# Optimization experiments

Measured on AMD Instinct MI355X. Metric: run time of the kernel, lower is better.

Reference implementation:

```python
import jax, jax.numpy as jnp
import numpy as np

B, C, H, W_SP = 16, 128, 28, 28
F, KS, STRIDE, PAD = 128, 3, 1, 1
CHUNK = 4      # filters per chunk for the L1 reduction (limits intermediate size)
EPS = 1e-12


def setup_inputs() -> dict:
    key = jax.random.key(0)
    kx, kw = jax.random.split(key)
    x = jax.random.normal(kx, (B, C, H, W_SP), dtype=jnp.float32)
    # kaiming_normal_: std = sqrt(2 / fan_in), fan_in = C*KS*KS
    std = float(np.sqrt(2.0 / (C * KS * KS)))
    W = jax.random.normal(kw, (F, C, KS, KS), dtype=jnp.float32) * std
    return {"x": x, "W": W}


def _patches(x):
    # im2col: [B, C*KS*KS, h_out, w_out], feature order (c, kh, kw) like torch unfold
    p = jax.lax.conv_general_dilated_patches(
        x, (KS, KS), (STRIDE, STRIDE), [(PAD, PAD), (PAD, PAD)],
        dimension_numbers=('NCHW', 'OIHW', 'NCHW'))
    b, k, ho, wo = p.shape
    return p.reshape(b, k, ho * wo), ho, wo


def reference(x, W):
    P, ho, wo = _patches(x)          # [B, K, L]
    Wc = W.reshape(F, -1)            # [F, K]
    K = Wc.shape[1]

    # Forward value: out = -cdist_L1(W, X_col) = -sum_k |W[f,k] - P[b,k,l]|
    # computed in filter chunks to avoid the full [F, K, B*L] diff tensor.
    Wch = Wc.reshape(F // CHUNK, CHUNK, K)
    def chunk_fn(wc):                # wc: [CHUNK, K]
        return jnp.sum(jnp.abs(wc[None, :, :, None] - P[:, None, :, :]), axis=2)  # [B, CHUNK, L]
    neg_l1 = -jax.lax.map(chunk_fn, Wch)                     # [F//CHUNK, B, CHUNK, L]
    neg_l1 = jnp.transpose(neg_l1, (1, 0, 2, 3)).reshape(P.shape[0], F, -1)  # [B, F, L]

    # Gradient path in original (straight-through): -cdist_L2, via GEMM decomposition.
    d2 = (jnp.sum(Wc * Wc, axis=1)[None, :, None]
          + jnp.sum(P * P, axis=1)[:, None, :]
          - 2.0 * jnp.einsum('fk,bkl->bfl', Wc, P))
    neg_l2 = -jnp.sqrt(jnp.maximum(d2, EPS))

    # value = -L1, gradient flows through -L2 (out.data = out_2.data in torch)
    out = neg_l2 + jax.lax.stop_gradient(neg_l1 - neg_l2)    # [B, F, L]
    return out.reshape(P.shape[0], F, ho, wo)
```

## Files before the change

### kernel.cpp

```cpp
#include <hip/hip_runtime.h>


#define B_    16
#define C_    128
#define HH    28
#define WW    28
#define F_    128
#define L_    (HH * WW)
#define K_    (C_ * 9)
#define M_    (B_ * L_)
#define TM    64
#define BC    4
#define KC    (BC * 9)
#define KP    (KC / 2)
#define SLAB  (B_ * F_ * L_)
#define NMT   (M_ / TM)
#define QS    4096.0f
#define QB    32768.5f

__device__ __forceinline__ unsigned sad16(unsigned a, unsigned b, unsigned c) {
    asm("v_sad_u16 %0, %1, %2, %0" : "+v"(c) : "v"(a), "v"(b));
    return c;
}

__global__ __launch_bounds__(256, 3)
void adder2d_main(const float* __restrict__ x, const float* __restrict__ Wg,
                  float* __restrict__ dst, int nch, int direct) {
    __shared__ __align__(16) unsigned Plq[2][KP][TM];
    __shared__ __align__(16) unsigned Wlq[2][KP][F_];

    const int t    = threadIdx.x;
    const int lane = t & 63;
    const int w    = t >> 6;
    const int tx   = lane & 7;
    const int ty   = lane >> 3;
    const int fw   = 32 * w;
    const int mt   = blockIdx.x, sp = blockIdx.z;
    const int c0   = sp * nch * BC;

    const int m  = mt * TM + lane;
    const int b  = m / L_;
    const int l  = m - b * L_;
    const int ho = l / WW, wo = l - ho * WW;
    int   toff[9];
    float sc[9];
    #pragma unroll
    for (int r = 0; r < 9; ++r) {
        const int dy = r / 3 - 1;
        const int dx = r - (r / 3) * 3 - 1;
        const bool ok = ((unsigned)(ho + dy) < (unsigned)HH) &&
                        ((unsigned)(wo + dx) < (unsigned)WW);
        toff[r] = ok ? (dy * WW + dx) : 0;
        sc[r]   = ok ? QS : 0.0f;
    }
    const float* xb = x + (size_t)b * (C_ * L_) + l;

    const int cp = w >> 1;
    const int r0 = (w & 1) ? 5 : 0;
    const int fW = t >> 1;
    const int pW = t & 1;
    const float* wbase = Wg + (size_t)fW * K_;

    unsigned acc[8][4];
    #pragma unroll
    for (int i = 0; i < 8; ++i)
        #pragma unroll
        for (int j = 0; j < 4; ++j) acc[i][j] = 0u;

    float ppre[10];
    float wpre[18];

    auto loadP = [&](int c8) {
        const float* x1 = xb + (size_t)(c8 + cp) * L_;
        const float* x2 = x1 + 2 * L_;
        #pragma unroll
        for (int i = 0; i < 5; ++i) {
            const int r  = r0 + i;
            const int rr = (r > 8) ? 8 : r;
            ppre[i]     = x1[toff[rr]];
            ppre[5 + i] = x2[toff[rr]];
        }
    };
    auto loadW = [&](int c8) {
        const float* w1 = wbase + (size_t)(c8 + pW) * 9;
        #pragma unroll
        for (int i = 0; i < 9; ++i) {
            wpre[i]     = w1[i];
            wpre[9 + i] = w1[18 + i];
        }
    };

    loadP(c0);
    loadW(c0);

    #pragma unroll 1
    for (int ch = 0; ch < nch; ++ch) {
        const int bufi = ch & 1;
        #pragma unroll
        for (int i = 0; i < 5; ++i) {
            const int r = r0 + i;
            if (r <= 8) {
                const unsigned qlo = (unsigned)__builtin_fmaf(ppre[i],     sc[r], QB);
                const unsigned qhi = (unsigned)__builtin_fmaf(ppre[5 + i], sc[r], QB);
                Plq[bufi][cp * 9 + r][lane] = (qlo & 0xffffu) | (qhi << 16);
            }
        }
        #pragma unroll
        for (int i = 0; i < 9; ++i) {
            const unsigned qlo = (unsigned)__builtin_fmaf(wpre[i],     QS, QB);
            const unsigned qhi = (unsigned)__builtin_fmaf(wpre[9 + i], QS, QB);
            Wlq[bufi][pW * 9 + i][fW] = (qlo & 0xffffu) | (qhi << 16);
        }
        if (ch + 1 < nch) {
            loadP(c0 + (ch + 1) * BC);
            loadW(c0 + (ch + 1) * BC);
        }
        asm volatile("s_waitcnt lgkmcnt(0)" ::: "memory");
        __builtin_amdgcn_s_barrier();
        asm volatile("" ::: "memory");
        __builtin_amdgcn_sched_barrier(0);
        #pragma unroll 6
        for (int kp = 0; kp < KP; ++kp) {
            const uint4 pA = *(const uint4*)&Plq[bufi][kp][tx * 8];
            const uint4 pB = *(const uint4*)&Plq[bufi][kp][tx * 8 + 4];
            const uint4 wA = *(const uint4*)&Wlq[bufi][kp][fw + ty * 4];
            const unsigned pm[8] = {pA.x, pA.y, pA.z, pA.w,
                                    pB.x, pB.y, pB.z, pB.w};
            const unsigned wn[4] = {wA.x, wA.y, wA.z, wA.w};
            #pragma unroll
            for (int i = 0; i < 8; ++i)
                #pragma unroll
                for (int j = 0; j < 4; ++j)
                    acc[i][j] = sad16(pm[i], wn[j], acc[i][j]);
        }
    }

    const int mb = mt * TM + tx * 8;
    const int bI = mb / L_;
    const int lb = mb - bI * L_;
    float* slab = direct ? dst : dst + (size_t)sp * SLAB;
    const float qs = (direct ? -1.0f : 1.0f) / QS;
    #pragma unroll
    for (int j = 0; j < 4; ++j) {
        const int f = fw + ty * 4 + j;
        float* o = &slab[(size_t)(bI * F_ + f) * L_ + lb];
        *(float4*)o       = make_float4(qs * (float)acc[0][j], qs * (float)acc[1][j],
                                        qs * (float)acc[2][j], qs * (float)acc[3][j]);
        *(float4*)(o + 4) = make_float4(qs * (float)acc[4][j], qs * (float)acc[5][j],
                                        qs * (float)acc[6][j], qs * (float)acc[7][j]);
    }
}

__global__ __launch_bounds__(256)
void adder2d_combine(const float* __restrict__ ws, float* __restrict__ out,
                     int nslab) {
    const int i = blockIdx.x * 256 + threadIdx.x;
    float4 r = make_float4(0.0f, 0.0f, 0.0f, 0.0f);
    for (int s = 0; s < nslab; ++s) {
        const float4 p = ((const float4*)(ws + (size_t)s * SLAB))[i];
        r.x += p.x; r.y += p.y; r.z += p.z; r.w += p.w;
    }
    ((float4*)out)[i] = make_float4(-r.x, -r.y, -r.z, -r.w);
}

extern "C" void kernel_launch(void* const* d_in, const int* in_sizes, int n_in,
                              void* d_out, int out_size, void* d_ws, size_t ws_size,
                              hipStream_t stream) {
    const float* x = (const float*)d_in[0];
    const float* W = (const float*)d_in[1];
    float* out = (float*)d_out;
    float* ws  = (float*)d_ws;

    int split = 0;
    if (ws_size >= (size_t)8 * SLAB * sizeof(float))      split = 8;
    else if (ws_size >= (size_t)4 * SLAB * sizeof(float)) split = 4;

    if (split) {
        dim3 grid(NMT, 1, split);
        adder2d_main<<<grid, 256, 0, stream>>>(x, W, ws, (C_ / BC) / split, 0);
        adder2d_combine<<<SLAB / 4 / 256, 256, 0, stream>>>(ws, out, split);
    } else {
        dim3 grid(NMT, 1, 1);
        adder2d_main<<<grid, 256, 0, stream>>>(x, W, out, C_ / BC, 1);
    }
}
```

Before: 113.4 us.

## Use 128-thread blocks with 8x8 per-thread SAD tiles and direct weight loads

Halves the block to two waves and has each thread accumulate an 8x8 tile instead of 8x4, so every LDS read of weights feeds twice as many SAD ops. Each thread now stages a full filter row per chunk with float4 global loads in the chunk loop, with no prefetch into registers. Patch staging now covers all 9 taps per wave. Register use roughly doubles and occupancy drops, and the weight loads are no longer overlapped with compute.

```diff
diff --git a/kernel.cpp b/kernel.cpp
--- a/kernel.cpp
+++ b/kernel.cpp
@@ -23,7 +23,7 @@
     return c;
 }
 
-__global__ __launch_bounds__(256, 3)
+__global__ __launch_bounds__(128, 2)
 void adder2d_main(const float* __restrict__ x, const float* __restrict__ Wg,
                   float* __restrict__ dst, int nch, int direct) {
     __shared__ __align__(16) unsigned Plq[2][KP][TM];
@@ -34,7 +34,7 @@
     const int w    = t >> 6;
     const int tx   = lane & 7;
     const int ty   = lane >> 3;
-    const int fw   = 32 * w;
+    const int fw   = 64 * w;
     const int mt   = blockIdx.x, sp = blockIdx.z;
     const int c0   = sp * nch * BC;
 
@@ -55,82 +55,76 @@
     }
     const float* xb = x + (size_t)b * (C_ * L_) + l;
 
-    const int cp = w >> 1;
-    const int r0 = (w & 1) ? 5 : 0;
-    const int fW = t >> 1;
-    const int pW = t & 1;
-    const float* wbase = Wg + (size_t)fW * K_;
+    const float* wrow = Wg + (size_t)t * K_;
 
-    unsigned acc[8][4];
+    unsigned acc[8][8];
     #pragma unroll
     for (int i = 0; i < 8; ++i)
         #pragma unroll
-        for (int j = 0; j < 4; ++j) acc[i][j] = 0u;
+        for (int j = 0; j < 8; ++j) acc[i][j] = 0u;
 
-    float ppre[10];
-    float wpre[18];
-
+    float ppre[18];
     auto loadP = [&](int c8) {
-        const float* x1 = xb + (size_t)(c8 + cp) * L_;
+        const float* x1 = xb + (size_t)(c8 + w) * L_;
         const float* x2 = x1 + 2 * L_;
         #pragma unroll
-        for (int i = 0; i < 5; ++i) {
-            const int r  = r0 + i;
-            const int rr = (r > 8) ? 8 : r;
-            ppre[i]     = x1[toff[rr]];
-            ppre[5 + i] = x2[toff[rr]];
-        }
-    };
-    auto loadW = [&](int c8) {
-        const float* w1 = wbase + (size_t)(c8 + pW) * 9;
-        #pragma unroll
-        for (int i = 0; i < 9; ++i) {
-            wpre[i]     = w1[i];
-            wpre[9 + i] = w1[18 + i];
+        for (int r = 0; r < 9; ++r) {
+            ppre[r]     = x1[toff[r]];
+            ppre[9 + r] = x2[toff[r]];
         }
     };
 
     loadP(c0);
-    loadW(c0);
 
     #pragma unroll 1
     for (int ch = 0; ch < nch; ++ch) {
         const int bufi = ch & 1;
+        const int c8 = c0 + ch * BC;
         #pragma unroll
-        for (int i = 0; i < 5; ++i) {
-            const int r = r0 + i;
-            if (r <= 8) {
-                const unsigned qlo = (unsigned)__builtin_fmaf(ppre[i],     sc[r], QB);
-                const unsigned qhi = (unsigned)__builtin_fmaf(ppre[5 + i], sc[r], QB);
-                Plq[bufi][cp * 9 + r][lane] = (qlo & 0xffffu) | (qhi << 16);
+        for (int r = 0; r < 9; ++r) {
+            const unsigned qlo = (unsigned)__builtin_fmaf(ppre[r],     sc[r], QB);
+            const unsigned qhi = (unsigned)__builtin_fmaf(ppre[9 + r], sc[r], QB);
+            Plq[bufi][w * 9 + r][lane] = (qlo & 0xffffu) | (qhi << 16);
+        }
+        {
+            const float4* wc = (const float4*)(wrow + (size_t)c8 * 9);
+            float wf[36];
+            #pragma unroll
+            for (int i = 0; i < 9; ++i) {
+                const float4 v = wc[i];
+                wf[4 * i + 0] = v.x; wf[4 * i + 1] = v.y;
+                wf[4 * i + 2] = v.z; wf[4 * i + 3] = v.w;
             }
+            #pragma unroll
+            for (int cp = 0; cp < 2; ++cp)
+                #pragma unroll
+                for (int r = 0; r < 9; ++r) {
+                    const unsigned qlo =
+                        (unsigned)__builtin_fmaf(wf[cp * 9 + r],      QS, QB);
+                    const unsigned qhi =
+                        (unsigned)__builtin_fmaf(wf[cp * 9 + r + 18], QS, QB);
+                    Wlq[bufi][cp * 9 + r][t] = (qlo & 0xffffu) | (qhi << 16);
+                }
         }
-        #pragma unroll
-        for (int i = 0; i < 9; ++i) {
-            const unsigned qlo = (unsigned)__builtin_fmaf(wpre[i],     QS, QB);
-            const unsigned qhi = (unsigned)__builtin_fmaf(wpre[9 + i], QS, QB);
-            Wlq[bufi][pW * 9 + i][fW] = (qlo & 0xffffu) | (qhi << 16);
-        }
-        if (ch + 1 < nch) {
-            loadP(c0 + (ch + 1) * BC);
-            loadW(c0 + (ch + 1) * BC);
-        }
+        if (ch + 1 < nch) loadP(c8 + BC);
         asm volatile("s_waitcnt lgkmcnt(0)" ::: "memory");
         __builtin_amdgcn_s_barrier();
         asm volatile("" ::: "memory");
         __builtin_amdgcn_sched_barrier(0);
-        #pragma unroll 6
+        #pragma unroll 3
         for (int kp = 0; kp < KP; ++kp) {
             const uint4 pA = *(const uint4*)&Plq[bufi][kp][tx * 8];
             const uint4 pB = *(const uint4*)&Plq[bufi][kp][tx * 8 + 4];
-            const uint4 wA = *(const uint4*)&Wlq[bufi][kp][fw + ty * 4];
+            const uint4 wA = *(const uint4*)&Wlq[bufi][kp][fw + ty * 8];
+            const uint4 wB = *(const uint4*)&Wlq[bufi][kp][fw + ty * 8 + 4];
             const unsigned pm[8] = {pA.x, pA.y, pA.z, pA.w,
                                     pB.x, pB.y, pB.z, pB.w};
-            const unsigned wn[4] = {wA.x, wA.y, wA.z, wA.w};
+            const unsigned wn[8] = {wA.x, wA.y, wA.z, wA.w,
+                                    wB.x, wB.y, wB.z, wB.w};
             #pragma unroll
             for (int i = 0; i < 8; ++i)
                 #pragma unroll
-                for (int j = 0; j < 4; ++j)
+                for (int j = 0; j < 8; ++j)
                     acc[i][j] = sad16(pm[i], wn[j], acc[i][j]);
         }
     }
@@ -141,8 +135,8 @@
     float* slab = direct ? dst : dst + (size_t)sp * SLAB;
     const float qs = (direct ? -1.0f : 1.0f) / QS;
     #pragma unroll
-    for (int j = 0; j < 4; ++j) {
-        const int f = fw + ty * 4 + j;
+    for (int j = 0; j < 8; ++j) {
+        const int f = fw + ty * 8 + j;
         float* o = &slab[(size_t)(bI * F_ + f) * L_ + lb];
         *(float4*)o       = make_float4(qs * (float)acc[0][j], qs * (float)acc[1][j],
                                         qs * (float)acc[2][j], qs * (float)acc[3][j]);
@@ -177,10 +171,10 @@
 
     if (split) {
         dim3 grid(NMT, 1, split);
-        adder2d_main<<<grid, 256, 0, stream>>>(x, W, ws, (C_ / BC) / split, 0);
+        adder2d_main<<<grid, 128, 0, stream>>>(x, W, ws, (C_ / BC) / split, 0);
         adder2d_combine<<<SLAB / 4 / 256, 256, 0, stream>>>(ws, out, split);
     } else {
         dim3 grid(NMT, 1, 1);
-        adder2d_main<<<grid, 256, 0, stream>>>(x, W, out, C_ / BC, 1);
+        adder2d_main<<<grid, 128, 0, stream>>>(x, W, out, C_ / BC, 1);
     }
 }
```

New measurement: 120.3 us. 6.1% more time.
